# Kernel tuning notes

Measured on AMD Instinct MI355X. Metric: run time of the kernel, lower is better.

## Reference

```python
import jax, jax.numpy as jnp
import numpy as np

CUTOFF = 5.0
N_GAUSS = 25
LOG2 = 0.6931471805599453
N_INTER = 3


def ssp(x):
    # shifted softplus used by SchNet
    return jax.nn.softplus(x) - LOG2


def setup_inputs() -> dict:
    key = jax.random.key(0)
    ks = jax.random.split(key, 16)
    B, A, N, F, G, Z = 16, 128, 127, 128, N_GAUSS, 100
    s = 1.0 / np.sqrt(F)
    emb = jax.random.normal(ks[0], (Z, F), jnp.float32)
    emb = emb.at[0].set(0.0)  # padding_idx=0
    inp = {
        "positions": jax.random.normal(ks[1], (B, A, 3), jnp.float32) * 3.0,
        "cell": jnp.zeros((B, 3, 3), jnp.float32),
        "cell_offset": jnp.zeros((B, A, N, 3), jnp.float32),
        "neighbor_mask": jnp.ones((B, A, N), jnp.float32),
        "embeddings": emb,
        "filt_W1": jax.random.normal(ks[2], (N_INTER, G, F), jnp.float32) / np.sqrt(G),
        "filt_b1": jnp.zeros((N_INTER, F), jnp.float32),
        "filt_W2": jax.random.normal(ks[3], (N_INTER, F, F), jnp.float32) * s,
        "filt_b2": jnp.zeros((N_INTER, F), jnp.float32),
        "in2f_W": jax.random.normal(ks[4], (N_INTER, F, F), jnp.float32) * s,
        "f2out_W": jax.random.normal(ks[5], (N_INTER, F, F), jnp.float32) * s,
        "f2out_b": jnp.zeros((N_INTER, F), jnp.float32),
        "dense_W": jax.random.normal(ks[6], (N_INTER, F, F), jnp.float32) * s,
        "dense_b": jnp.zeros((N_INTER, F), jnp.float32),
        "atomic_numbers": jax.random.randint(ks[7], (B, A), 1, Z).astype(jnp.int32),
        "neighbors": jax.random.randint(ks[8], (B, A, N), 0, A).astype(jnp.int32),
    }
    return inp


def _schnet_forward(positions, cell, cell_offset, neighbor_mask, embeddings,
                    filt_W1, filt_b1, filt_W2, filt_b2,
                    in2f_W, f2out_W, f2out_b, dense_W, dense_b,
                    atomic_numbers, neighbors):
    B, A, _ = positions.shape
    bidx = jnp.arange(B)[:, None, None]

    # ---- AtomDistances: gather neighbor positions, pairwise distances ----
    pos_nbh = positions[bidx, neighbors]            # [B,A,N,3]
    dvec = pos_nbh - positions[:, :, None, :]
    dvec = dvec + jnp.einsum('banj,bjc->banc', cell_offset, cell)
    d2 = jnp.sum(dvec * dvec, axis=-1)              # [B,A,N]
    m = neighbor_mask > 0
    r_ij = jnp.where(m, jnp.sqrt(jnp.where(m, d2, 1.0)), 0.0)

    # ---- GaussianSmearing(0, cutoff, 25) ----
    centers = jnp.linspace(0.0, CUTOFF, N_GAUSS, dtype=r_ij.dtype)
    width = centers[1] - centers[0]
    coeff = -0.5 / (width * width)
    diff = r_ij[..., None] - centers                # [B,A,N,G]
    f_ij = jnp.exp(coeff * diff * diff)

    # ---- CosineCutoff ----
    C = 0.5 * (jnp.cos(r_ij * jnp.pi / CUTOFF) + 1.0)
    C = C * (r_ij < CUTOFF).astype(r_ij.dtype)      # [B,A,N]

    # ---- embedding ----
    x = embeddings[atomic_numbers]                  # [B,A,F]

    # ---- interaction blocks (cfconv + dense residual) ----
    for l in range(N_INTER):
        W = ssp(jnp.einsum('bang,gf->banf', f_ij, filt_W1[l]) + filt_b1[l])
        W = jnp.einsum('banf,fg->bang', W, filt_W2[l]) + filt_b2[l]
        W = W * C[..., None]                        # [B,A,N,F]
        y = x @ in2f_W[l]                           # [B,A,F], no bias
        y_nbh = y[bidx, neighbors]                  # [B,A,N,F]
        agg = jnp.sum(y_nbh * W * neighbor_mask[..., None], axis=2)  # [B,A,F]
        v = ssp(agg @ f2out_W[l] + f2out_b[l])
        v = v @ dense_W[l] + dense_b[l]
        x = x + v
    return x


def reference(positions, cell, cell_offset, neighbor_mask, embeddings,
              filt_W1, filt_b1, filt_W2, filt_b2,
              in2f_W, f2out_W, f2out_b, dense_W, dense_b,
              atomic_numbers, neighbors):
    return _schnet_forward(positions, cell, cell_offset, neighbor_mask, embeddings,
                           filt_W1, filt_b1, filt_W2, filt_b2,
                           in2f_W, f2out_W, f2out_b, dense_W, dense_b,
                           atomic_numbers, neighbors)
```

## Files before the change

### kernel.cpp

```cpp
#include <hip/hip_runtime.h>
#include <math.h>

#define BB 16
#define AA 128
#define NNB 127
#define FF 128
#define GG 25

typedef __attribute__((ext_vector_type(8))) short bf16x8;
typedef __attribute__((ext_vector_type(4))) float f32x4;
typedef unsigned short ushort_t;

__device__ __forceinline__ float ssp_f(float x) {
    return fmaxf(x, 0.f) + log1pf(__expf(-fabsf(x))) - 0.6931471805599453f;
}

__device__ __forceinline__ float ssp_fast(float x) {
    float e = __expf(-fabsf(x));
    float p = fmaf(e, 0.03215845f, -0.13606275f);
    p = fmaf(e, p, 0.28947478f);
    p = fmaf(e, p, -0.49190896f);
    p = fmaf(e, p, 0.99949556f);
    return fmaxf(x, 0.f) + e * p - 0.6931471805599453f;
}

__device__ __forceinline__ ushort_t f2bf(float f) {
    unsigned int u = __float_as_uint(f);
    unsigned int r = (u + 0x7fffu + ((u >> 16) & 1u)) >> 16;
    return (ushort_t)r;
}

__device__ __forceinline__ float bf2f(ushort_t h) {
    return __uint_as_float(((unsigned int)h) << 16);
}

__device__ __forceinline__ unsigned int pack2bf_rhu(float lo, float hi) {
    return __builtin_amdgcn_perm(__float_as_uint(hi) + 0x8000u,
                                 __float_as_uint(lo) + 0x8000u, 0x07060302u);
}

__device__ __forceinline__ int yperm(int f) {
    return (f & ~31) + ((f & 15) << 1) + ((f >> 4) & 1);
}

__global__ __launch_bounds__(256) void k_setup(
    const float* __restrict__ positions, const float* __restrict__ cell,
    const float* __restrict__ cell_offset, const float* __restrict__ nmask,
    const int* __restrict__ neighbors,
    const float* __restrict__ W1, const float* __restrict__ W2,
    const float* __restrict__ Win, const float* __restrict__ Wf, const float* __restrict__ Wd,
    const float* __restrict__ emb, const int* __restrict__ z,
    float* __restrict__ r_g, float* __restrict__ cm_g,
    ushort_t* __restrict__ w1t, ushort_t* __restrict__ w2f,
    ushort_t* __restrict__ whi, ushort_t* __restrict__ wlo,
    float* __restrict__ x) {
    int i = blockIdx.x * 256 + threadIdx.x;
    if (i < BB * AA * 128) {
        int row = i >> 7, n = i & 127;
        if (n < NNB) {
            int b = row >> 7;
            int nb = neighbors[row * NNB + n];
            float px = positions[row * 3 + 0], py = positions[row * 3 + 1], pz = positions[row * 3 + 2];
            int nrow = b * AA + nb;
            float qx = positions[nrow * 3 + 0], qy = positions[nrow * 3 + 1], qz = positions[nrow * 3 + 2];
            const float* co = cell_offset + (size_t)row * NNB * 3 + (size_t)n * 3;
            const float* cl = cell + b * 9;
            float c0 = co[0], c1 = co[1], c2 = co[2];
            float ox = c0 * cl[0] + c1 * cl[3] + c2 * cl[6];
            float oy = c0 * cl[1] + c1 * cl[4] + c2 * cl[7];
            float oz = c0 * cl[2] + c1 * cl[5] + c2 * cl[8];
            float dx = qx - px + ox, dy = qy - py + oy, dz = qz - pz + oz;
            float d2 = dx * dx + dy * dy + dz * dz;
            float mk = nmask[row * NNB + n];
            float r = (mk > 0.f) ? sqrtf(d2) : 0.f;
            float Cc = 0.5f * (__cosf(r * (3.14159265358979323846f / 5.0f)) + 1.f);
            Cc = (r < 5.0f) ? Cc : 0.f;
            r_g[i] = r;
            cm_g[i] = Cc * mk;
        } else {
            r_g[i] = 1e9f;
            cm_g[i] = 0.f;
        }
        int f = i & 127;
        x[i] = emb[z[i >> 7] * FF + f];
    }
    if (i < 3 * 128 * 32) {
        int l = i >> 12, rem = i & 4095, f = rem >> 5, g = rem & 31;
        float v = (g < GG) ? W1[l * GG * FF + g * FF + f] : 0.f;
        w1t[i] = f2bf(v);
    }
    if (i < 3 * 16384) {
        int l = i >> 14, e = i & 16383;
        int u = e >> 3, j = e & 7;
        int ks = u >> 9, rem = u & 511;
        int wcft = rem >> 6, lane = rem & 63;
        int f = (wcft >> 1) * 32 + (wcft & 1) * 16 + (lane & 15);
        int k = ks * 32 + (lane >> 4) * 8 + j;
        w2f[i] = f2bf(W2[l * 16384 + k * 128 + f]);
    }
    if (i < 9 * 16384) {
        int m = i / 49152;
        int rem = i - m * 49152;
        int l = rem >> 14;
        int rk = rem & 16383;
        int f = rk >> 7, k = rk & 127;
        const float* src = (m == 0) ? Win : ((m == 1) ? Wf : Wd);
        float v = src[l * 16384 + k * 128 + f];
        ushort_t h = f2bf(v);
        whi[i] = h;
        wlo[i] = f2bf(v - bf2f(h));
    }
}

__global__ __launch_bounds__(512) void k_ffn(
    const float* __restrict__ agg, const float* __restrict__ x_in,
    float* __restrict__ x_out, float* __restrict__ y, float* __restrict__ out,
    const ushort_t* __restrict__ wfh, const ushort_t* __restrict__ wfl, const float* __restrict__ bfv_g,
    const ushort_t* __restrict__ wdh, const ushort_t* __restrict__ wdl, const float* __restrict__ bdv_g,
    const ushort_t* __restrict__ wih, const ushort_t* __restrict__ wil,
    int mode) {
    __shared__ ushort_t tsh[8][136];
    __shared__ ushort_t tsl[8][136];
    const int t = threadIdx.x;
    const int lane = t & 63, w = t >> 6;
    const int l15 = lane & 15, l4 = lane >> 4;
    const int r0 = blockIdx.x << 3;
    const int fcol = (w << 4) + l15;

    bf16x8 Ah[4], Al[4];

    auto loadA_global = [&](const float* __restrict__ M) {
#pragma unroll
        for (int ks = 0; ks < 4; ++ks) {
            float v[8];
            if (l15 < 8) {
                const float4* p = (const float4*)(M + ((size_t)(r0 + l15) << 7) + (ks << 5) + (l4 << 3));
                float4 a = p[0], b = p[1];
                v[0] = a.x; v[1] = a.y; v[2] = a.z; v[3] = a.w;
                v[4] = b.x; v[5] = b.y; v[6] = b.z; v[7] = b.w;
            } else {
#pragma unroll
                for (int j = 0; j < 8; ++j) v[j] = 0.f;
            }
#pragma unroll
            for (int j = 0; j < 8; ++j) {
                ushort_t h = f2bf(v[j]);
                Ah[ks][j] = (short)h;
                Al[ks][j] = (short)f2bf(v[j] - bf2f(h));
            }
        }
    };
    auto loadA_lds = [&]() {
#pragma unroll
        for (int ks = 0; ks < 4; ++ks) {
            if (l15 < 8) {
                const char* base = (const char*)&tsh[l15][0] + (ks << 6) + (l4 << 4);
                Ah[ks] = *(const bf16x8*)base;
                const char* basel = (const char*)&tsl[l15][0] + (ks << 6) + (l4 << 4);
                Al[ks] = *(const bf16x8*)basel;
            } else {
#pragma unroll
                for (int j = 0; j < 8; ++j) { Ah[ks][j] = 0; Al[ks][j] = 0; }
            }
        }
    };

    if (mode & 1) {
        loadA_global(agg);
        float bfv = bfv_g[fcol];
        f32x4 acc = {bfv, bfv, bfv, bfv};
#pragma unroll
        for (int ks = 0; ks < 4; ++ks) {
            const bf16x8 Bh = *(const bf16x8*)(wfh + ((size_t)fcol << 7) + (ks << 5) + (l4 << 3));
            const bf16x8 Bl = *(const bf16x8*)(wfl + ((size_t)fcol << 7) + (ks << 5) + (l4 << 3));
            acc = __builtin_amdgcn_mfma_f32_16x16x32_bf16(Al[ks], Bh, acc, 0, 0, 0);
            acc = __builtin_amdgcn_mfma_f32_16x16x32_bf16(Ah[ks], Bl, acc, 0, 0, 0);
            acc = __builtin_amdgcn_mfma_f32_16x16x32_bf16(Ah[ks], Bh, acc, 0, 0, 0);
        }
#pragma unroll
        for (int reg = 0; reg < 4; ++reg) {
            int r = (l4 << 2) + reg;
            if (r < 8) {
                float v = ssp_f(acc[reg]);
                ushort_t h = f2bf(v);
                tsh[r][fcol] = h;
                tsl[r][fcol] = f2bf(v - bf2f(h));
            }
        }
        __syncthreads();
        loadA_lds();
        float bdv = bdv_g[fcol];
        f32x4 acc2 = {bdv, bdv, bdv, bdv};
#pragma unroll
        for (int ks = 0; ks < 4; ++ks) {
            const bf16x8 Bh = *(const bf16x8*)(wdh + ((size_t)fcol << 7) + (ks << 5) + (l4 << 3));
            const bf16x8 Bl = *(const bf16x8*)(wdl + ((size_t)fcol << 7) + (ks << 5) + (l4 << 3));
            acc2 = __builtin_amdgcn_mfma_f32_16x16x32_bf16(Al[ks], Bh, acc2, 0, 0, 0);
            acc2 = __builtin_amdgcn_mfma_f32_16x16x32_bf16(Ah[ks], Bl, acc2, 0, 0, 0);
            acc2 = __builtin_amdgcn_mfma_f32_16x16x32_bf16(Ah[ks], Bh, acc2, 0, 0, 0);
        }
        __syncthreads();
#pragma unroll
        for (int reg = 0; reg < 4; ++reg) {
            int r = (l4 << 2) + reg;
            if (r < 8) {
                size_t gi = ((size_t)(r0 + r) << 7) + fcol;
                float xn = x_in[gi] + acc2[reg];
                x_out[gi] = xn;
                if (mode & 4) out[gi] = xn;
                if (mode & 2) {
                    ushort_t h = f2bf(xn);
                    tsh[r][fcol] = h;
                    tsl[r][fcol] = f2bf(xn - bf2f(h));
                }
            }
        }
        if (mode & 2) __syncthreads();
    }
    if (mode & 2) {
        if (mode & 1) loadA_lds(); else loadA_global(x_in);
        f32x4 acc3 = {0.f, 0.f, 0.f, 0.f};
#pragma unroll
        for (int ks = 0; ks < 4; ++ks) {
            const bf16x8 Bh = *(const bf16x8*)(wih + ((size_t)fcol << 7) + (ks << 5) + (l4 << 3));
            const bf16x8 Bl = *(const bf16x8*)(wil + ((size_t)fcol << 7) + (ks << 5) + (l4 << 3));
            acc3 = __builtin_amdgcn_mfma_f32_16x16x32_bf16(Al[ks], Bh, acc3, 0, 0, 0);
            acc3 = __builtin_amdgcn_mfma_f32_16x16x32_bf16(Ah[ks], Bl, acc3, 0, 0, 0);
            acc3 = __builtin_amdgcn_mfma_f32_16x16x32_bf16(Ah[ks], Bh, acc3, 0, 0, 0);
        }
        const int pf = yperm(fcol);
#pragma unroll
        for (int reg = 0; reg < 4; ++reg) {
            int r = (l4 << 2) + reg;
            if (r < 8) y[((size_t)(r0 + r) << 7) + pf] = acc3[reg];
        }
    }
}

#define SMEM_BYTES 33792

__global__ __launch_bounds__(512, 6) void k_cfconv(
    const float* __restrict__ r_g, const float* __restrict__ cm_g,
    const int* __restrict__ neighbors,
    const ushort_t* __restrict__ w1t, const float* __restrict__ b1,
    const ushort_t* __restrict__ w2f, const float* __restrict__ b2,
    const float* __restrict__ y, float* __restrict__ agg) {
    extern __shared__ char smem[];
    float* cm_s = (float*)(smem + 32768);
    int* nbr_s = (int*)(smem + 33280);
    float* red_s = (float*)smem;

    const int row = blockIdx.x;
    const int b = row >> 7;
    const int t = threadIdx.x;
    const int lane = t & 63, w = t >> 6;
    const int l15 = lane & 15, l4 = lane >> 4;
    const int wr = w >> 2, wc = w & 3;

    if (t < 128) {
        cm_s[t] = cm_g[((size_t)row << 7) + t];
        nbr_s[t] = (t < NNB) ? neighbors[row * NNB + t] : 0;
    }

    {
        const int nrow = (w << 4) + l15;
        const float rv = r_g[((size_t)row << 7) + nrow];
        const float width = 5.0f / (GG - 1);
        const float coeff = -0.5f / (width * width);
        float fv[8];
#pragma unroll
        for (int j = 0; j < 8; ++j) {
            int g = (l4 << 3) + j;
            float d = rv - g * width;
            fv[j] = (g < GG) ? __expf(coeff * d * d) : 0.f;
        }
        bf16x8 fb;
        unsigned int* fbu = (unsigned int*)&fb;
        fbu[0] = pack2bf_rhu(fv[0], fv[1]);
        fbu[1] = pack2bf_rhu(fv[2], fv[3]);
        fbu[2] = pack2bf_rhu(fv[4], fv[5]);
        fbu[3] = pack2bf_rhu(fv[6], fv[7]);
        const int base = nrow * 256;
        const int sw = (nrow & 7) << 4;
#pragma unroll
        for (int ft = 0; ft < 8; ++ft) {
            bf16x8 aw = *(const bf16x8*)(w1t + ((ft << 4) + l15) * 32 + (l4 << 3));
            const int f0 = (ft << 4) + (l4 << 2);
            f32x4 c0 = *(const f32x4*)(b1 + f0);
            f32x4 d = __builtin_amdgcn_mfma_f32_16x16x32_bf16(aw, fb, c0, 0, 0, 0);
            unsigned int lo32 = pack2bf_rhu(ssp_fast(d[0]), ssp_fast(d[1]));
            unsigned int hi32 = pack2bf_rhu(ssp_fast(d[2]), ssp_fast(d[3]));
            unsigned long long pk = (unsigned long long)lo32 | ((unsigned long long)hi32 << 32);
            *(unsigned long long*)(smem + base + ((f0 << 1) ^ sw)) = pk;
        }
    }

#define W2LD(ks, ft) (*(const bf16x8*)(w2f + (((((ks) << 3) + (wc << 1) + (ft)) << 6) + lane) * 8))
    bf16x8 wb0 = W2LD(0, 0), wb1 = W2LD(0, 1);
    __syncthreads();

    f32x4 acc[4][2];
#pragma unroll
    for (int mi = 0; mi < 4; ++mi)
#pragma unroll
        for (int ft = 0; ft < 2; ++ft) {
            float b2v = b2[(wc << 5) + (ft << 4) + l15];
            f32x4 c0 = {b2v, b2v, b2v, b2v};
            acc[mi][ft] = c0;
        }
#pragma unroll
    for (int ks = 0; ks < 4; ++ks) {
        bf16x8 wn0, wn1;
        if (ks < 3) { wn0 = W2LD(ks + 1, 0); wn1 = W2LD(ks + 1, 1); }
        bf16x8 ha[4];
#pragma unroll
        for (int mi = 0; mi < 4; ++mi) {
            int n = (wr << 6) + (mi << 4) + l15;
            ha[mi] = *(const bf16x8*)(smem + n * 256 + ((((ks << 2) + l4) << 4) ^ ((n & 7) << 4)));
        }
#pragma unroll
        for (int mi = 0; mi < 4; ++mi) {
            acc[mi][0] = __builtin_amdgcn_mfma_f32_16x16x32_bf16(ha[mi], wb0, acc[mi][0], 0, 0, 0);
            acc[mi][1] = __builtin_amdgcn_mfma_f32_16x16x32_bf16(ha[mi], wb1, acc[mi][1], 0, 0, 0);
        }
        if (ks < 3) { wb0 = wn0; wb1 = wn1; }
    }
#undef W2LD
    __syncthreads();

    float part0 = 0.f, part1 = 0.f;
    const float* ybase = y + ((size_t)(b * AA) << 7) + (wc << 5) + (l15 << 1);
#pragma unroll
    for (int mi = 0; mi < 4; ++mi) {
        int n0 = (wr << 6) + (mi << 4) + (l4 << 2);
        float4 cmv = *(const float4*)(cm_s + n0);
        int4 nb4 = *(const int4*)(nbr_s + n0);
        float2 y0 = *(const float2*)(ybase + ((size_t)nb4.x << 7));
        float2 y1 = *(const float2*)(ybase + ((size_t)nb4.y << 7));
        float2 y2 = *(const float2*)(ybase + ((size_t)nb4.z << 7));
        float2 y3 = *(const float2*)(ybase + ((size_t)nb4.w << 7));
        part0 = fmaf(y0.x, acc[mi][0][0] * cmv.x, part0);
        part1 = fmaf(y0.y, acc[mi][1][0] * cmv.x, part1);
        part0 = fmaf(y1.x, acc[mi][0][1] * cmv.y, part0);
        part1 = fmaf(y1.y, acc[mi][1][1] * cmv.y, part1);
        part0 = fmaf(y2.x, acc[mi][0][2] * cmv.z, part0);
        part1 = fmaf(y2.y, acc[mi][1][2] * cmv.z, part1);
        part0 = fmaf(y3.x, acc[mi][0][3] * cmv.w, part0);
        part1 = fmaf(y3.y, acc[mi][1][3] * cmv.w, part1);
    }
    {
        int xg = l4 << 3;
        red_s[(w << 7) + (l4 << 5) + (l15 ^ xg)] = part0;
        red_s[(w << 7) + (l4 << 5) + ((16 + l15) ^ xg)] = part1;
    }
    __syncthreads();
    if (t < FF) {
        int wcf = t >> 5, fl = t & 31;
        float s = 0.f;
#pragma unroll
        for (int wr2 = 0; wr2 < 2; ++wr2)
#pragma unroll
            for (int g = 0; g < 4; ++g)
                s += red_s[(((wr2 << 2) + wcf) << 7) + (g << 5) + (fl ^ (g << 3))];
        agg[(size_t)row * FF + t] = s;
    }
}

extern "C" void kernel_launch(void* const* d_in, const int* in_sizes, int n_in,
                              void* d_out, int out_size, void* d_ws, size_t ws_size,
                              hipStream_t stream) {
    const float* positions   = (const float*)d_in[0];
    const float* cell        = (const float*)d_in[1];
    const float* cell_offset = (const float*)d_in[2];
    const float* nmask       = (const float*)d_in[3];
    const float* emb         = (const float*)d_in[4];
    const float* filt_W1     = (const float*)d_in[5];
    const float* filt_b1     = (const float*)d_in[6];
    const float* filt_W2     = (const float*)d_in[7];
    const float* filt_b2     = (const float*)d_in[8];
    const float* in2f_W      = (const float*)d_in[9];
    const float* f2out_W     = (const float*)d_in[10];
    const float* f2out_b     = (const float*)d_in[11];
    const float* dense_W     = (const float*)d_in[12];
    const float* dense_b     = (const float*)d_in[13];
    const int* atomic_numbers = (const int*)d_in[14];
    const int* neighbors      = (const int*)d_in[15];
    float* out = (float*)d_out;

    float* x    = (float*)d_ws;
    float* yb   = x + BB * AA * FF;
    float* agg  = yb + BB * AA * FF;
    float* r_g  = agg + BB * AA * FF;
    float* cm_g = r_g + BB * AA * 128;
    ushort_t* w1t = (ushort_t*)(cm_g + BB * AA * 128);
    ushort_t* w2f = w1t + 3 * 128 * 32;
    ushort_t* whi = w2f + 3 * 16384;
    ushort_t* wlo = whi + 9 * 16384;

    k_setup<<<1024, 256, 0, stream>>>(positions, cell, cell_offset, nmask, neighbors,
                                      filt_W1, filt_W2, in2f_W, f2out_W, dense_W,
                                      emb, atomic_numbers,
                                      r_g, cm_g, w1t, w2f, whi, wlo, x);

    k_ffn<<<256, 512, 0, stream>>>(x, x, x, yb, out,
                                   whi + 3 * 16384, wlo + 3 * 16384, f2out_b,
                                   whi + 6 * 16384, wlo + 6 * 16384, dense_b,
                                   whi + 0 * 16384, wlo + 0 * 16384,
                                   2);
    for (int l = 0; l < 3; ++l) {
        k_cfconv<<<BB * AA, 512, SMEM_BYTES, stream>>>(
            r_g, cm_g, neighbors,
            w1t + (size_t)l * 128 * 32, filt_b1 + (size_t)l * FF,
            w2f + (size_t)l * 16384, filt_b2 + (size_t)l * FF,
            yb, agg);
        int nextl = (l < 2) ? (l + 1) : 0;
        int mode = 1 | ((l < 2) ? 2 : 0) | ((l == 2) ? 4 : 0);
        k_ffn<<<256, 512, 0, stream>>>(agg, x, x, yb, out,
                                       whi + (3 + l) * 16384, wlo + (3 + l) * 16384, f2out_b + (size_t)l * FF,
                                       whi + (6 + l) * 16384, wlo + (6 + l) * 16384, dense_b + (size_t)l * FF,
                                       whi + nextl * 16384, wlo + nextl * 16384,
                                       mode);
    }
}
```

Baseline: 129.8 us.

## Process two atom rows per cfconv block, keeping filter weights in registers

```diff
diff --git a/kernel.cpp b/kernel.cpp
--- a/kernel.cpp
+++ b/kernel.cpp
@@ -10,6 +10,10 @@
 typedef __attribute__((ext_vector_type(8))) short bf16x8;
 typedef __attribute__((ext_vector_type(4))) float f32x4;
 typedef unsigned short ushort_t;
+
+#define GLOBAL_LOAD_LDS16(gp, lp)                                                        \
+    __builtin_amdgcn_global_load_lds((const __attribute__((address_space(1))) unsigned int*)(gp), \
+                                     (__attribute__((address_space(3))) unsigned int*)(lp), 16, 0, 0)
 
 __device__ __forceinline__ float ssp_f(float x) {
     return fmaxf(x, 0.f) + log1pf(__expf(-fabsf(x))) - 0.6931471805599453f;
@@ -237,7 +241,7 @@
     }
 }
 
-#define SMEM_BYTES 33792
+#define SMEM_BYTES 47104
 
 __global__ __launch_bounds__(512, 6) void k_cfconv(
     const float* __restrict__ r_g, const float* __restrict__ cm_g,
@@ -246,123 +250,135 @@
     const ushort_t* __restrict__ w2f, const float* __restrict__ b2,
     const float* __restrict__ y, float* __restrict__ agg) {
     extern __shared__ char smem[];
-    float* cm_s = (float*)(smem + 32768);
-    int* nbr_s = (int*)(smem + 33280);
-    float* red_s = (float*)smem;
-
-    const int row = blockIdx.x;
-    const int b = row >> 7;
+    float* red_s = (float*)(smem + 32768);
+    float* cm_s = (float*)(smem + 45056);
+    int* nbr_s = (int*)(smem + 46080);
+
+    const int row0 = blockIdx.x << 1;
+    const int b = row0 >> 7;
     const int t = threadIdx.x;
     const int lane = t & 63, w = t >> 6;
     const int l15 = lane & 15, l4 = lane >> 4;
     const int wr = w >> 2, wc = w & 3;
 
-    if (t < 128) {
-        cm_s[t] = cm_g[((size_t)row << 7) + t];
-        nbr_s[t] = (t < NNB) ? neighbors[row * NNB + t] : 0;
-    }
-
-    {
-        const int nrow = (w << 4) + l15;
-        const float rv = r_g[((size_t)row << 7) + nrow];
-        const float width = 5.0f / (GG - 1);
-        const float coeff = -0.5f / (width * width);
-        float fv[8];
-#pragma unroll
-        for (int j = 0; j < 8; ++j) {
-            int g = (l4 << 3) + j;
-            float d = rv - g * width;
-            fv[j] = (g < GG) ? __expf(coeff * d * d) : 0.f;
-        }
-        bf16x8 fb;
-        unsigned int* fbu = (unsigned int*)&fb;
-        fbu[0] = pack2bf_rhu(fv[0], fv[1]);
-        fbu[1] = pack2bf_rhu(fv[2], fv[3]);
-        fbu[2] = pack2bf_rhu(fv[4], fv[5]);
-        fbu[3] = pack2bf_rhu(fv[6], fv[7]);
-        const int base = nrow * 256;
-        const int sw = (nrow & 7) << 4;
-#pragma unroll
-        for (int ft = 0; ft < 8; ++ft) {
-            bf16x8 aw = *(const bf16x8*)(w1t + ((ft << 4) + l15) * 32 + (l4 << 3));
-            const int f0 = (ft << 4) + (l4 << 2);
-            f32x4 c0 = *(const f32x4*)(b1 + f0);
-            f32x4 d = __builtin_amdgcn_mfma_f32_16x16x32_bf16(aw, fb, c0, 0, 0, 0);
-            unsigned int lo32 = pack2bf_rhu(ssp_fast(d[0]), ssp_fast(d[1]));
-            unsigned int hi32 = pack2bf_rhu(ssp_fast(d[2]), ssp_fast(d[3]));
-            unsigned long long pk = (unsigned long long)lo32 | ((unsigned long long)hi32 << 32);
-            *(unsigned long long*)(smem + base + ((f0 << 1) ^ sw)) = pk;
-        }
-    }
-
-#define W2LD(ks, ft) (*(const bf16x8*)(w2f + (((((ks) << 3) + (wc << 1) + (ft)) << 6) + lane) * 8))
-    bf16x8 wb0 = W2LD(0, 0), wb1 = W2LD(0, 1);
+    GLOBAL_LOAD_LDS16((const char*)w1t + (w << 10) + (lane << 4), smem + 36864 + (w << 10));
+
+    bf16x8 w2r[8];
+#pragma unroll
+    for (int ks = 0; ks < 4; ++ks) {
+#pragma unroll
+        for (int ft = 0; ft < 2; ++ft)
+            w2r[(ks << 1) + ft] = *(const bf16x8*)(w2f + ((((ks << 3) + (wc << 1) + ft) << 6) + lane) * 8);
+    }
+    f32x4 b1r[8];
+#pragma unroll
+    for (int ft = 0; ft < 8; ++ft) b1r[ft] = *(const f32x4*)(b1 + (ft << 4) + (l4 << 2));
+    const float b2v0 = b2[(wc << 5) + l15];
+    const float b2v1 = b2[(wc << 5) + 16 + l15];
+
+    if (t < 256) {
+        int a = t >> 7, n = t & 127;
+        cm_s[(a << 7) + n] = cm_g[((size_t)(row0 + a) << 7) + n];
+        nbr_s[(a << 7) + n] = (n < NNB) ? neighbors[(row0 + a) * NNB + n] : 0;
+    }
     __syncthreads();
 
-    f32x4 acc[4][2];
-#pragma unroll
-    for (int mi = 0; mi < 4; ++mi)
-#pragma unroll
-        for (int ft = 0; ft < 2; ++ft) {
-            float b2v = b2[(wc << 5) + (ft << 4) + l15];
-            f32x4 c0 = {b2v, b2v, b2v, b2v};
-            acc[mi][ft] = c0;
-        }
-#pragma unroll
-    for (int ks = 0; ks < 4; ++ks) {
-        bf16x8 wn0, wn1;
-        if (ks < 3) { wn0 = W2LD(ks + 1, 0); wn1 = W2LD(ks + 1, 1); }
-        bf16x8 ha[4];
+#pragma unroll
+    for (int a = 0; a < 2; ++a) {
+        const int row = row0 + a;
+        {
+            const int nrow = (w << 4) + l15;
+            const float rv = r_g[((size_t)row << 7) + nrow];
+            const float width = 5.0f / (GG - 1);
+            const float coeff = -0.5f / (width * width);
+            float fv[8];
+#pragma unroll
+            for (int j = 0; j < 8; ++j) {
+                int g = (l4 << 3) + j;
+                float d = rv - g * width;
+                fv[j] = (g < GG) ? __expf(coeff * d * d) : 0.f;
+            }
+            bf16x8 fb;
+            unsigned int* fbu = (unsigned int*)&fb;
+            fbu[0] = pack2bf_rhu(fv[0], fv[1]);
+            fbu[1] = pack2bf_rhu(fv[2], fv[3]);
+            fbu[2] = pack2bf_rhu(fv[4], fv[5]);
+            fbu[3] = pack2bf_rhu(fv[6], fv[7]);
+            const int base = nrow * 256;
+            const int sw = (nrow & 7) << 4;
+#pragma unroll
+            for (int ft = 0; ft < 8; ++ft) {
+                bf16x8 aw = *(const bf16x8*)(smem + 36864 + ((((ft << 4) + l15)) << 6) + (l4 << 4));
+                const int f0 = (ft << 4) + (l4 << 2);
+                f32x4 d = __builtin_amdgcn_mfma_f32_16x16x32_bf16(aw, fb, b1r[ft], 0, 0, 0);
+                unsigned int lo32 = pack2bf_rhu(ssp_fast(d[0]), ssp_fast(d[1]));
+                unsigned int hi32 = pack2bf_rhu(ssp_fast(d[2]), ssp_fast(d[3]));
+                unsigned long long pk = (unsigned long long)lo32 | ((unsigned long long)hi32 << 32);
+                *(unsigned long long*)(smem + base + ((f0 << 1) ^ sw)) = pk;
+            }
+        }
+        __syncthreads();
+
+        f32x4 acc[4][2];
 #pragma unroll
         for (int mi = 0; mi < 4; ++mi) {
-            int n = (wr << 6) + (mi << 4) + l15;
-            ha[mi] = *(const bf16x8*)(smem + n * 256 + ((((ks << 2) + l4) << 4) ^ ((n & 7) << 4)));
-        }
+            f32x4 c00 = {b2v0, b2v0, b2v0, b2v0};
+            f32x4 c01 = {b2v1, b2v1, b2v1, b2v1};
+            acc[mi][0] = c00;
+            acc[mi][1] = c01;
+        }
+#pragma unroll
+        for (int ks = 0; ks < 4; ++ks) {
+            bf16x8 ha[4];
+#pragma unroll
+            for (int mi = 0; mi < 4; ++mi) {
+                int n = (wr << 6) + (mi << 4) + l15;
+                ha[mi] = *(const bf16x8*)(smem + n * 256 + ((((ks << 2) + l4) << 4) ^ ((n & 7) << 4)));
+            }
+#pragma unroll
+            for (int mi = 0; mi < 4; ++mi) {
+                acc[mi][0] = __builtin_amdgcn_mfma_f32_16x16x32_bf16(ha[mi], w2r[(ks << 1)], acc[mi][0], 0, 0, 0);
+                acc[mi][1] = __builtin_amdgcn_mfma_f32_16x16x32_bf16(ha[mi], w2r[(ks << 1) + 1], acc[mi][1], 0, 0, 0);
+            }
+        }
+        __syncthreads();
+
+        float part0 = 0.f, part1 = 0.f;
+        const float* ybase = y + ((size_t)(b * AA) << 7) + (wc << 5) + (l15 << 1);
 #pragma unroll
         for (int mi = 0; mi < 4; ++mi) {
-            acc[mi][0] = __builtin_amdgcn_mfma_f32_16x16x32_bf16(ha[mi], wb0, acc[mi][0], 0, 0, 0);
-            acc[mi][1] = __builtin_amdgcn_mfma_f32_16x16x32_bf16(ha[mi], wb1, acc[mi][1], 0, 0, 0);
-        }
-        if (ks < 3) { wb0 = wn0; wb1 = wn1; }
-    }
-#undef W2LD
-    __syncthreads();
-
-    float part0 = 0.f, part1 = 0.f;
-    const float* ybase = y + ((size_t)(b * AA) << 7) + (wc << 5) + (l15 << 1);
-#pragma unroll
-    for (int mi = 0; mi < 4; ++mi) {
-        int n0 = (wr << 6) + (mi << 4) + (l4 << 2);
-        float4 cmv = *(const float4*)(cm_s + n0);
-        int4 nb4 = *(const int4*)(nbr_s + n0);
-        float2 y0 = *(const float2*)(ybase + ((size_t)nb4.x << 7));
-        float2 y1 = *(const float2*)(ybase + ((size_t)nb4.y << 7));
-        float2 y2 = *(const float2*)(ybase + ((size_t)nb4.z << 7));
-        float2 y3 = *(const float2*)(ybase + ((size_t)nb4.w << 7));
-        part0 = fmaf(y0.x, acc[mi][0][0] * cmv.x, part0);
-        part1 = fmaf(y0.y, acc[mi][1][0] * cmv.x, part1);
-        part0 = fmaf(y1.x, acc[mi][0][1] * cmv.y, part0);
-        part1 = fmaf(y1.y, acc[mi][1][1] * cmv.y, part1);
-        part0 = fmaf(y2.x, acc[mi][0][2] * cmv.z, part0);
-        part1 = fmaf(y2.y, acc[mi][1][2] * cmv.z, part1);
-        part0 = fmaf(y3.x, acc[mi][0][3] * cmv.w, part0);
-        part1 = fmaf(y3.y, acc[mi][1][3] * cmv.w, part1);
-    }
-    {
-        int xg = l4 << 3;
-        red_s[(w << 7) + (l4 << 5) + (l15 ^ xg)] = part0;
-        red_s[(w << 7) + (l4 << 5) + ((16 + l15) ^ xg)] = part1;
-    }
-    __syncthreads();
-    if (t < FF) {
-        int wcf = t >> 5, fl = t & 31;
-        float s = 0.f;
-#pragma unroll
-        for (int wr2 = 0; wr2 < 2; ++wr2)
-#pragma unroll
-            for (int g = 0; g < 4; ++g)
-                s += red_s[(((wr2 << 2) + wcf) << 7) + (g << 5) + (fl ^ (g << 3))];
-        agg[(size_t)row * FF + t] = s;
+            int n0 = (wr << 6) + (mi << 4) + (l4 << 2);
+            float4 cmv = *(const float4*)(cm_s + (a << 7) + n0);
+            int4 nb4 = *(const int4*)(nbr_s + (a << 7) + n0);
+            float2 y0 = *(const float2*)(ybase + ((size_t)nb4.x << 7));
+            float2 y1 = *(const float2*)(ybase + ((size_t)nb4.y << 7));
+            float2 y2 = *(const float2*)(ybase + ((size_t)nb4.z << 7));
+            float2 y3 = *(const float2*)(ybase + ((size_t)nb4.w << 7));
+            part0 = fmaf(y0.x, acc[mi][0][0] * cmv.x, part0);
+            part1 = fmaf(y0.y, acc[mi][1][0] * cmv.x, part1);
+            part0 = fmaf(y1.x, acc[mi][0][1] * cmv.y, part0);
+            part1 = fmaf(y1.y, acc[mi][1][1] * cmv.y, part1);
+            part0 = fmaf(y2.x, acc[mi][0][2] * cmv.z, part0);
+            part1 = fmaf(y2.y, acc[mi][1][2] * cmv.z, part1);
+            part0 = fmaf(y3.x, acc[mi][0][3] * cmv.w, part0);
+            part1 = fmaf(y3.y, acc[mi][1][3] * cmv.w, part1);
+        }
+        {
+            int xg = l4 << 3;
+            red_s[(w << 7) + (l4 << 5) + (l15 ^ xg)] = part0;
+            red_s[(w << 7) + (l4 << 5) + ((16 + l15) ^ xg)] = part1;
+        }
+        __syncthreads();
+        if (t < FF) {
+            int wcf = t >> 5, fl = t & 31;
+            float s = 0.f;
+#pragma unroll
+            for (int wr2 = 0; wr2 < 2; ++wr2)
+#pragma unroll
+                for (int g = 0; g < 4; ++g)
+                    s += red_s[(((wr2 << 2) + wcf) << 7) + (g << 5) + (fl ^ (g << 3))];
+            agg[(size_t)row * FF + t] = s;
+        }
     }
 }
 
@@ -408,7 +424,7 @@
                                    whi + 0 * 16384, wlo + 0 * 16384,
                                    2);
     for (int l = 0; l < 3; ++l) {
-        k_cfconv<<<BB * AA, 512, SMEM_BYTES, stream>>>(
+        k_cfconv<<<BB * AA / 2, 512, SMEM_BYTES, stream>>>(
             r_g, cm_g, neighbors,
             w1t + (size_t)l * 128 * 32, filt_b1 + (size_t)l * FF,
             w2f + (size_t)l * 16384, filt_b2 + (size_t)l * FF,
```

After: 292.5 us. 2.25x slower.

## Split cfconv neighbors across two blocks and sum partial aggregates in ffn

Applied to the files above, without the earlier changes.

```diff
diff --git a/kernel.cpp b/kernel.cpp
--- a/kernel.cpp
+++ b/kernel.cpp
@@ -37,10 +37,6 @@
 __device__ __forceinline__ unsigned int pack2bf_rhu(float lo, float hi) {
     return __builtin_amdgcn_perm(__float_as_uint(hi) + 0x8000u,
                                  __float_as_uint(lo) + 0x8000u, 0x07060302u);
-}
-
-__device__ __forceinline__ int yperm(int f) {
-    return (f & ~31) + ((f & 15) << 1) + ((f >> 4) & 1);
 }
 
 __global__ __launch_bounds__(256) void k_setup(
@@ -113,7 +109,8 @@
 }
 
 __global__ __launch_bounds__(512) void k_ffn(
-    const float* __restrict__ agg, const float* __restrict__ x_in,
+    const float* __restrict__ agg0, const float* __restrict__ agg1,
+    const float* __restrict__ x_in,
     float* __restrict__ x_out, float* __restrict__ y, float* __restrict__ out,
     const ushort_t* __restrict__ wfh, const ushort_t* __restrict__ wfl, const float* __restrict__ bfv_g,
     const ushort_t* __restrict__ wdh, const ushort_t* __restrict__ wdl, const float* __restrict__ bdv_g,
@@ -129,35 +126,59 @@
 
     bf16x8 Ah[4], Al[4];
 
+    auto splitA = [&](float* v) {
+#pragma unroll
+        for (int ks = 0; ks < 4; ++ks)
+#pragma unroll
+            for (int j = 0; j < 8; ++j) {
+                float vv = v[ks * 8 + j];
+                ushort_t h = f2bf(vv);
+                Ah[ks][j] = (short)h;
+                Al[ks][j] = (short)f2bf(vv - bf2f(h));
+            }
+    };
     auto loadA_global = [&](const float* __restrict__ M) {
-#pragma unroll
-        for (int ks = 0; ks < 4; ++ks) {
-            float v[8];
+        float v[32];
+#pragma unroll
+        for (int ks = 0; ks < 4; ++ks) {
             if (l15 < 8) {
                 const float4* p = (const float4*)(M + ((size_t)(r0 + l15) << 7) + (ks << 5) + (l4 << 3));
-                float4 a = p[0], b = p[1];
-                v[0] = a.x; v[1] = a.y; v[2] = a.z; v[3] = a.w;
-                v[4] = b.x; v[5] = b.y; v[6] = b.z; v[7] = b.w;
+                float4 a = p[0], c = p[1];
+                v[ks * 8 + 0] = a.x; v[ks * 8 + 1] = a.y; v[ks * 8 + 2] = a.z; v[ks * 8 + 3] = a.w;
+                v[ks * 8 + 4] = c.x; v[ks * 8 + 5] = c.y; v[ks * 8 + 6] = c.z; v[ks * 8 + 7] = c.w;
             } else {
 #pragma unroll
-                for (int j = 0; j < 8; ++j) v[j] = 0.f;
-            }
-#pragma unroll
-            for (int j = 0; j < 8; ++j) {
-                ushort_t h = f2bf(v[j]);
-                Ah[ks][j] = (short)h;
-                Al[ks][j] = (short)f2bf(v[j] - bf2f(h));
-            }
-        }
+                for (int j = 0; j < 8; ++j) v[ks * 8 + j] = 0.f;
+            }
+        }
+        splitA(v);
+    };
+    auto loadA_sum = [&](const float* __restrict__ M, const float* __restrict__ M2) {
+        float v[32];
+#pragma unroll
+        for (int ks = 0; ks < 4; ++ks) {
+            if (l15 < 8) {
+                size_t off = ((size_t)(r0 + l15) << 7) + (ks << 5) + (l4 << 3);
+                const float4* p = (const float4*)(M + off);
+                const float4* q = (const float4*)(M2 + off);
+                float4 a = p[0], c = p[1], a2 = q[0], c2 = q[1];
+                v[ks * 8 + 0] = a.x + a2.x; v[ks * 8 + 1] = a.y + a2.y;
+                v[ks * 8 + 2] = a.z + a2.z; v[ks * 8 + 3] = a.w + a2.w;
+                v[ks * 8 + 4] = c.x + c2.x; v[ks * 8 + 5] = c.y + c2.y;
+                v[ks * 8 + 6] = c.z + c2.z; v[ks * 8 + 7] = c.w + c2.w;
+            } else {
+#pragma unroll
+                for (int j = 0; j < 8; ++j) v[ks * 8 + j] = 0.f;
+            }
+        }
+        splitA(v);
     };
     auto loadA_lds = [&]() {
 #pragma unroll
         for (int ks = 0; ks < 4; ++ks) {
             if (l15 < 8) {
-                const char* base = (const char*)&tsh[l15][0] + (ks << 6) + (l4 << 4);
-                Ah[ks] = *(const bf16x8*)base;
-                const char* basel = (const char*)&tsl[l15][0] + (ks << 6) + (l4 << 4);
-                Al[ks] = *(const bf16x8*)basel;
+                Ah[ks] = *(const bf16x8*)((const char*)&tsh[l15][0] + (ks << 6) + (l4 << 4));
+                Al[ks] = *(const bf16x8*)((const char*)&tsl[l15][0] + (ks << 6) + (l4 << 4));
             } else {
 #pragma unroll
                 for (int j = 0; j < 8; ++j) { Ah[ks][j] = 0; Al[ks][j] = 0; }
@@ -166,7 +187,7 @@
     };
 
     if (mode & 1) {
-        loadA_global(agg);
+        loadA_sum(agg0, agg1);
         float bfv = bfv_g[fcol];
         f32x4 acc = {bfv, bfv, bfv, bfv};
 #pragma unroll
@@ -228,141 +249,118 @@
             acc3 = __builtin_amdgcn_mfma_f32_16x16x32_bf16(Ah[ks], Bl, acc3, 0, 0, 0);
             acc3 = __builtin_amdgcn_mfma_f32_16x16x32_bf16(Ah[ks], Bh, acc3, 0, 0, 0);
         }
-        const int pf = yperm(fcol);
 #pragma unroll
         for (int reg = 0; reg < 4; ++reg) {
             int r = (l4 << 2) + reg;
-            if (r < 8) y[((size_t)(r0 + r) << 7) + pf] = acc3[reg];
-        }
-    }
-}
-
-#define SMEM_BYTES 33792
-
-__global__ __launch_bounds__(512, 6) void k_cfconv(
+            if (r < 8) y[((size_t)(r0 + r) << 7) + fcol] = acc3[reg];
+        }
+    }
+}
+
+#define SMEM_BYTES 22016
+
+__global__ __launch_bounds__(512, 4) void k_cfconv(
     const float* __restrict__ r_g, const float* __restrict__ cm_g,
     const int* __restrict__ neighbors,
     const ushort_t* __restrict__ w1t, const float* __restrict__ b1,
     const ushort_t* __restrict__ w2f, const float* __restrict__ b2,
-    const float* __restrict__ y, float* __restrict__ agg) {
+    const float* __restrict__ y,
+    float* __restrict__ agg0, float* __restrict__ agg1) {
     extern __shared__ char smem[];
-    float* cm_s = (float*)(smem + 32768);
-    int* nbr_s = (int*)(smem + 33280);
-    float* red_s = (float*)smem;
-
-    const int row = blockIdx.x;
+    float* cm_s = (float*)(smem + 21504);
+    int* nbr_s = (int*)(smem + 21760);
+
+    const int bid = blockIdx.x;
+    const int row = bid >> 1;
+    const int hh = bid & 1;
     const int b = row >> 7;
     const int t = threadIdx.x;
     const int lane = t & 63, w = t >> 6;
     const int l15 = lane & 15, l4 = lane >> 4;
-    const int wr = w >> 2, wc = w & 3;
-
-    if (t < 128) {
-        cm_s[t] = cm_g[((size_t)row << 7) + t];
-        nbr_s[t] = (t < NNB) ? neighbors[row * NNB + t] : 0;
-    }
-
+
+    bf16x8 w2r[4];
+#pragma unroll
+    for (int ks = 0; ks < 4; ++ks)
+        w2r[ks] = *(const bf16x8*)(w2f + ((((ks << 3) + w) << 6) + lane) * 8);
+    const bf16x8 aw = *(const bf16x8*)(w1t + ((w << 4) + l15) * 32 + (l4 << 3));
+    const f32x4 b1v = *(const f32x4*)(b1 + (w << 4) + (l4 << 2));
+    const float b2v = b2[(w << 4) + l15];
+
+    if (t < 64) {
+        int ng = (hh << 6) + t;
+        cm_s[t] = cm_g[((size_t)row << 7) + ng];
+        nbr_s[t] = (ng < NNB) ? neighbors[row * NNB + ng] : 0;
+    }
     {
-        const int nrow = (w << 4) + l15;
-        const float rv = r_g[((size_t)row << 7) + nrow];
+        int nl = t >> 3, g0 = (t & 7) << 2;
+        float rv = r_g[((size_t)row << 7) + (hh << 6) + nl];
         const float width = 5.0f / (GG - 1);
         const float coeff = -0.5f / (width * width);
-        float fv[8];
-#pragma unroll
-        for (int j = 0; j < 8; ++j) {
-            int g = (l4 << 3) + j;
+        float v[4];
+#pragma unroll
+        for (int j = 0; j < 4; ++j) {
+            int g = g0 + j;
             float d = rv - g * width;
-            fv[j] = (g < GG) ? __expf(coeff * d * d) : 0.f;
-        }
-        bf16x8 fb;
-        unsigned int* fbu = (unsigned int*)&fb;
-        fbu[0] = pack2bf_rhu(fv[0], fv[1]);
-        fbu[1] = pack2bf_rhu(fv[2], fv[3]);
-        fbu[2] = pack2bf_rhu(fv[4], fv[5]);
-        fbu[3] = pack2bf_rhu(fv[6], fv[7]);
-        const int base = nrow * 256;
-        const int sw = (nrow & 7) << 4;
-#pragma unroll
-        for (int ft = 0; ft < 8; ++ft) {
-            bf16x8 aw = *(const bf16x8*)(w1t + ((ft << 4) + l15) * 32 + (l4 << 3));
-            const int f0 = (ft << 4) + (l4 << 2);
-            f32x4 c0 = *(const f32x4*)(b1 + f0);
-            f32x4 d = __builtin_amdgcn_mfma_f32_16x16x32_bf16(aw, fb, c0, 0, 0, 0);
+            v[j] = (g < GG) ? __expf(coeff * d * d) : 0.f;
+        }
+        unsigned long long pk = (unsigned long long)pack2bf_rhu(v[0], v[1])
+            | ((unsigned long long)pack2bf_rhu(v[2], v[3]) << 32);
+        *(unsigned long long*)(smem + 16384 + nl * 80 + (g0 << 1)) = pk;
+    }
+    __syncthreads();
+
+    {
+        bf16x8 fb[4];
+#pragma unroll
+        for (int ng = 0; ng < 4; ++ng)
+            fb[ng] = *(const bf16x8*)(smem + 16384 + ((ng << 4) + l15) * 80 + (l4 << 4));
+        const int f0 = (w << 4) + (l4 << 2);
+#pragma unroll
+        for (int ng = 0; ng < 4; ++ng) {
+            f32x4 d = __builtin_amdgcn_mfma_f32_16x16x32_bf16(aw, fb[ng], b1v, 0, 0, 0);
+            int nl = (ng << 4) + l15;
             unsigned int lo32 = pack2bf_rhu(ssp_fast(d[0]), ssp_fast(d[1]));
             unsigned int hi32 = pack2bf_rhu(ssp_fast(d[2]), ssp_fast(d[3]));
             unsigned long long pk = (unsigned long long)lo32 | ((unsigned long long)hi32 << 32);
-            *(unsigned long long*)(smem + base + ((f0 << 1) ^ sw)) = pk;
-        }
-    }
-
-#define W2LD(ks, ft) (*(const bf16x8*)(w2f + (((((ks) << 3) + (wc << 1) + (ft)) << 6) + lane) * 8))
-    bf16x8 wb0 = W2LD(0, 0), wb1 = W2LD(0, 1);
+            *(unsigned long long*)(smem + nl * 256 + ((f0 << 1) ^ ((nl & 7) << 4))) = pk;
+        }
+    }
     __syncthreads();
 
-    f32x4 acc[4][2];
-#pragma unroll
-    for (int mi = 0; mi < 4; ++mi)
-#pragma unroll
-        for (int ft = 0; ft < 2; ++ft) {
-            float b2v = b2[(wc << 5) + (ft << 4) + l15];
-            f32x4 c0 = {b2v, b2v, b2v, b2v};
-            acc[mi][ft] = c0;
-        }
+    f32x4 acc[4];
+#pragma unroll
+    for (int mi = 0; mi < 4; ++mi) {
+        f32x4 c = {b2v, b2v, b2v, b2v};
+        acc[mi] = c;
+    }
 #pragma unroll
     for (int ks = 0; ks < 4; ++ks) {
-        bf16x8 wn0, wn1;
-        if (ks < 3) { wn0 = W2LD(ks + 1, 0); wn1 = W2LD(ks + 1, 1); }
-        bf16x8 ha[4];
 #pragma unroll
         for (int mi = 0; mi < 4; ++mi) {
-            int n = (wr << 6) + (mi << 4) + l15;
-            ha[mi] = *(const bf16x8*)(smem + n * 256 + ((((ks << 2) + l4) << 4) ^ ((n & 7) << 4)));
-        }
-#pragma unroll
-        for (int mi = 0; mi < 4; ++mi) {
-            acc[mi][0] = __builtin_amdgcn_mfma_f32_16x16x32_bf16(ha[mi], wb0, acc[mi][0], 0, 0, 0);
-            acc[mi][1] = __builtin_amdgcn_mfma_f32_16x16x32_bf16(ha[mi], wb1, acc[mi][1], 0, 0, 0);
-        }
-        if (ks < 3) { wb0 = wn0; wb1 = wn1; }
-    }
-#undef W2LD
-    __syncthreads();
-
-    float part0 = 0.f, part1 = 0.f;
-    const float* ybase = y + ((size_t)(b * AA) << 7) + (wc << 5) + (l15 << 1);
+            int nl = (mi << 4) + l15;
+            bf16x8 ha = *(const bf16x8*)(smem + nl * 256 + ((((ks << 2) + l4) << 4) ^ ((nl & 7) << 4)));
+            acc[mi] = __builtin_amdgcn_mfma_f32_16x16x32_bf16(ha, w2r[ks], acc[mi], 0, 0, 0);
+        }
+    }
+
+    float part = 0.f;
+    const int f = (w << 4) + l15;
+    const float* yb2 = y + ((size_t)(b * AA) << 7) + f;
 #pragma unroll
     for (int mi = 0; mi < 4; ++mi) {
-        int n0 = (wr << 6) + (mi << 4) + (l4 << 2);
+        int n0 = (mi << 4) + (l4 << 2);
         float4 cmv = *(const float4*)(cm_s + n0);
         int4 nb4 = *(const int4*)(nbr_s + n0);
-        float2 y0 = *(const float2*)(ybase + ((size_t)nb4.x << 7));
-        float2 y1 = *(const float2*)(ybase + ((size_t)nb4.y << 7));
-        float2 y2 = *(const float2*)(ybase + ((size_t)nb4.z << 7));
-        float2 y3 = *(const float2*)(ybase + ((size_t)nb4.w << 7));
-        part0 = fmaf(y0.x, acc[mi][0][0] * cmv.x, part0);
-        part1 = fmaf(y0.y, acc[mi][1][0] * cmv.x, part1);
-        part0 = fmaf(y1.x, acc[mi][0][1] * cmv.y, part0);
-        part1 = fmaf(y1.y, acc[mi][1][1] * cmv.y, part1);
-        part0 = fmaf(y2.x, acc[mi][0][2] * cmv.z, part0);
-        part1 = fmaf(y2.y, acc[mi][1][2] * cmv.z, part1);
-        part0 = fmaf(y3.x, acc[mi][0][3] * cmv.w, part0);
-        part1 = fmaf(y3.y, acc[mi][1][3] * cmv.w, part1);
-    }
-    {
-        int xg = l4 << 3;
-        red_s[(w << 7) + (l4 << 5) + (l15 ^ xg)] = part0;
-        red_s[(w << 7) + (l4 << 5) + ((16 + l15) ^ xg)] = part1;
-    }
-    __syncthreads();
-    if (t < FF) {
-        int wcf = t >> 5, fl = t & 31;
-        float s = 0.f;
-#pragma unroll
-        for (int wr2 = 0; wr2 < 2; ++wr2)
-#pragma unroll
-            for (int g = 0; g < 4; ++g)
-                s += red_s[(((wr2 << 2) + wcf) << 7) + (g << 5) + (fl ^ (g << 3))];
-        agg[(size_t)row * FF + t] = s;
+        part = fmaf(yb2[(size_t)nb4.x << 7], acc[mi][0] * cmv.x, part);
+        part = fmaf(yb2[(size_t)nb4.y << 7], acc[mi][1] * cmv.y, part);
+        part = fmaf(yb2[(size_t)nb4.z << 7], acc[mi][2] * cmv.z, part);
+        part = fmaf(yb2[(size_t)nb4.w << 7], acc[mi][3] * cmv.w, part);
+    }
+    part += __shfl_xor(part, 16);
+    part += __shfl_xor(part, 32);
+    if (l4 == 0) {
+        float* aggp = hh ? agg1 : agg0;
+        aggp[((size_t)row << 7) + f] = part;
     }
 }
 
@@ -389,8 +387,9 @@
 
     float* x    = (float*)d_ws;
     float* yb   = x + BB * AA * FF;
-    float* agg  = yb + BB * AA * FF;
-    float* r_g  = agg + BB * AA * FF;
+    float* agg0 = yb + BB * AA * FF;
+    float* agg1 = agg0 + BB * AA * FF;
+    float* r_g  = agg1 + BB * AA * FF;
     float* cm_g = r_g + BB * AA * 128;
     ushort_t* w1t = (ushort_t*)(cm_g + BB * AA * 128);
     ushort_t* w2f = w1t + 3 * 128 * 32;
@@ -402,20 +401,20 @@
                                       emb, atomic_numbers,
                                       r_g, cm_g, w1t, w2f, whi, wlo, x);
 
-    k_ffn<<<256, 512, 0, stream>>>(x, x, x, yb, out,
+    k_ffn<<<256, 512, 0, stream>>>(x, x, x, x, yb, out,
                                    whi + 3 * 16384, wlo + 3 * 16384, f2out_b,
                                    whi + 6 * 16384, wlo + 6 * 16384, dense_b,
                                    whi + 0 * 16384, wlo + 0 * 16384,
                                    2);
     for (int l = 0; l < 3; ++l) {
-        k_cfconv<<<BB * AA, 512, SMEM_BYTES, stream>>>(
+        k_cfconv<<<BB * AA * 2, 512, SMEM_BYTES, stream>>>(
             r_g, cm_g, neighbors,
             w1t + (size_t)l * 128 * 32, filt_b1 + (size_t)l * FF,
             w2f + (size_t)l * 16384, filt_b2 + (size_t)l * FF,
-            yb, agg);
+            yb, agg0, agg1);
         int nextl = (l < 2) ? (l + 1) : 0;
         int mode = 1 | ((l < 2) ? 2 : 0) | ((l == 2) ? 4 : 0);
-        k_ffn<<<256, 512, 0, stream>>>(agg, x, x, yb, out,
+        k_ffn<<<256, 512, 0, stream>>>(agg0, agg1, x, x, yb, out,
                                        whi + (3 + l) * 16384, wlo + (3 + l) * 16384, f2out_b + (size_t)l * FF,
                                        whi + (6 + l) * 16384, wlo + (6 + l) * 16384, dense_b + (size_t)l * FF,
                                        whi + nextl * 16384, wlo + nextl * 16384,
```

Result: slower. 133.4 us (+2.8%).
